# Performance work log

Measured on AMD Instinct MI355X. Metric: run time of the kernel, lower is better.

The kernel has to match this reference:

```python
import jax, jax.numpy as jnp
import numpy as np

BZ = 512      # number of graph pairs
NMAX = 128    # max nodes per graph (pad size; original uses sz.max())
D = 64        # node feature dim
EPS = 1e-3    # sinkhorn entropic regularization (from forward: 0.001)
ITERS = 500   # max_iters (reference runs the full budget, no early stop)
NEG = -1e5    # log(0) surrogate, safe in fp32


def setup_inputs() -> dict:
    key = jax.random.key(0)
    k1, k2, k3, k4 = jax.random.split(key, 4)
    x1 = jax.random.normal(k1, (BZ * NMAX, D), dtype=jnp.float32)
    x2 = jax.random.normal(k2, (BZ * NMAX, D), dtype=jnp.float32)
    # graph sizes in [64, 128] so no empty graphs
    sz1 = jax.random.randint(k3, (BZ,), 64, NMAX + 1, dtype=jnp.int32)
    sz2 = jax.random.randint(k4, (BZ,), 64, NMAX + 1, dtype=jnp.int32)
    return {"x1": x1, "x2": x2, "sz1": sz1, "sz2": sz2}


def _pack(x, sz, nmax):
    """Ragged [total,d] -> padded [bz,nmax,d] plus float mask [bz,nmax].
    Vectorized equivalent of the python packing loop in forward()."""
    off = jnp.cumsum(sz) - sz                       # exclusive prefix sum
    idx = off[:, None] + jnp.arange(nmax)[None, :]  # [bz, nmax]
    mask = jnp.arange(nmax)[None, :] < sz[:, None]
    g = x[jnp.clip(idx, 0, x.shape[0] - 1)] * mask[..., None].astype(x.dtype)
    return g, mask.astype(x.dtype)


def _pairwise_sq(s1, s2):
    """pairwise_distances(set1, set2, p=2): squared euclidean cost [bz,n1,n2]."""
    n1 = jnp.sum(s1 * s1, axis=-1)
    n2 = jnp.sum(s2 * s2, axis=-1)
    M = n1[:, :, None] + n2[:, None, :] - 2.0 * jnp.einsum('bnd,bmd->bnm', s1, s2)
    return jnp.maximum(M, 0.0)


def _sinkhorn(a, b, M, eps, iters):
    """Log-domain entropic Sinkhorn; padded rows/cols have a,b == 0 and
    receive NEG potentials so their transport mass is exp(NEG) ~ 0."""
    la = jnp.where(a > 0, jnp.log(jnp.where(a > 0, a, 1.0)), NEG)
    lb = jnp.where(b > 0, jnp.log(jnp.where(b > 0, b, 1.0)), NEG)
    logK = -M / eps                                  # [bz, n1, n2]

    def body(_, uv):
        u, v = uv
        v = lb - jax.scipy.special.logsumexp(logK + u[:, :, None], axis=1)
        u = la - jax.scipy.special.logsumexp(logK + v[:, None, :], axis=2)
        return (u, v)

    u0 = jnp.zeros_like(a)
    v0 = jnp.zeros_like(b)
    u, v = jax.lax.fori_loop(0, iters, body, (u0, v0))
    return jnp.exp(logK + u[:, :, None] + v[:, None, :])


def reference(x1, x2, sz1, sz2):
    set1, a = _pack(x1, sz1, NMAX)      # [bz, NMAX, D], [bz, NMAX]
    set2, bm = _pack(x2, sz2, NMAX)
    # b = b * a.sum(1,keepdim) / b.sum(1,keepdim)
    b = bm * a.sum(1, keepdims=True) / bm.sum(1, keepdims=True)
    M = _pairwise_sq(set1, set2)
    # original passes M.detach() to sinkhorn -> P is constant w.r.t. grads
    P = _sinkhorn(a, b, jax.lax.stop_gradient(M), EPS, ITERS)
    return jnp.sum(M * P, axis=(1, 2))  # [bz]
```

## Files before the change

### kernel.cpp

```cpp
#include <hip/hip_runtime.h>

#ifndef __has_builtin
#define __has_builtin(x) 0
#endif

typedef float v2f __attribute__((ext_vector_type(2)));

__device__ __forceinline__ float fexp2(float x) {
#if __has_builtin(__builtin_amdgcn_exp2f)
    return __builtin_amdgcn_exp2f(x);
#else
    return exp2f(x);
#endif
}
__device__ __forceinline__ float flog2(float x) {
#if __has_builtin(__builtin_amdgcn_logf)
    return __builtin_amdgcn_logf(x);
#else
    return log2f(x);
#endif
}
__device__ __forceinline__ float frcp(float x) {
#if __has_builtin(__builtin_amdgcn_rcpf)
    return __builtin_amdgcn_rcpf(x);
#else
    return 1.0f / x;
#endif
}

#define DPP_QX1  0xB1
#define DPP_QX2  0x4E
#define DPP_ROR4 0x124
#define DPP_ROR8 0x128

template<int CTRL>
__device__ __forceinline__ float dppf(float x) {
    return __int_as_float(__builtin_amdgcn_update_dpp(
        0, __float_as_int(x), CTRL, 0xF, 0xF, true));
}
__device__ __forceinline__ float swzx16(float x) {
    return __int_as_float(__builtin_amdgcn_ds_swizzle(__float_as_int(x), 0x401F));
}

__device__ __forceinline__ float sel4(float a0, float a1, float a2, float a3,
                                      bool c1, bool c2) {
    float x = c1 ? a1 : a0;
    float y = c1 ? a3 : a2;
    return c2 ? y : x;
}

#define NMAXN 128
#define DD    64
#define MAX_ITERS 500
#define KLOG  12

#define NEG2  (-144269.50408889634f)
#define LKSC  (-1442.6950408889634f)
#define OUTSC (-6.931471805599453e-4f)

#define LK(r, c) (((c) & 1) ? lk2[r][(c) >> 1].y : lk2[r][(c) >> 1].x)

struct SmemStage {
    float A[NMAXN * 33];
    float B[NMAXN * 33];
    float nA[NMAXN];
    float nB[NMAXN];
};
struct SmemSink {
    float2 plog[NMAXN * 10];
    float  ulog[NMAXN];
    float  pmul[NMAXN * 9];
    float  g[NMAXN];
};
union SmemU {
    SmemStage st;
    SmemSink  sk;
    char force[61440];
};

__global__ __launch_bounds__(512, 1)
void balance_kernel(const int* __restrict__ sz1, int* __restrict__ perm)
{
    __shared__ int keys[512];
    const int tid = threadIdx.x;
    const int k = sz1[tid];
    keys[tid] = k;
    __syncthreads();
    int r = 0;
    for (int j = 0; j < 512; ++j) {
        const int kj = keys[j];
        r += (int)((kj < k) | ((kj == k) & (j < tid)));
    }
    const int p = (r < 256) ? r : (767 - r);
    perm[p] = tid;
}

template<int NR>
__device__ __forceinline__ float sink_mul(
    v2f (&lk2)[8][2], const float (&uloc)[8], const float (&v)[4],
    const float (&fm)[4], float gmask,
    SmemU& sm, int rg, int cg, int w, int crow, int q)
{
    const bool c1 = (cg & 1) != 0;
    const bool c2 = (cg & 2) != 0;
    const int  pstoreL = (rg + 16 * cg) * 9 + w;
    const int  pstoreH = pstoreL + 576;

    v2f Q2[NR][2];
#pragma unroll
    for (int r = 0; r < NR; ++r)
#pragma unroll
        for (int j = 0; j < 2; ++j) {
            Q2[r][j].x = fexp2(LK(r, 2*j    ) + uloc[r] + v[2*j    ]);
            Q2[r][j].y = fexp2(LK(r, 2*j + 1) + uloc[r] + v[2*j + 1]);
        }
    float gl[NR];
#pragma unroll
    for (int r = 0; r < NR; ++r) gl[r] = 1.f;
    v2f fc2[2];
    fc2[0].x = fc2[0].y = 0.f;
    fc2[1] = fc2[0];

    for (int k = KLOG; k < MAX_ITERS; ++k) {
        v2f p0 = Q2[0][0] * gl[0];
        v2f q0 = Q2[0][1] * gl[0];
        v2f p1; p1.x = 0.f; p1.y = 0.f;
        v2f q1 = p1;
        if constexpr (NR > 1) { p1 = Q2[1][0] * gl[1]; q1 = Q2[1][1] * gl[1]; }
#pragma unroll
        for (int r = 2; r < NR; ++r) {
            if ((r & 1) == 0) { p0 += Q2[r][0] * gl[r]; q0 += Q2[r][1] * gl[r]; }
            else              { p1 += Q2[r][0] * gl[r]; q1 += Q2[r][1] * gl[r]; }
        }
        v2f s20 = p0 + p1;
        v2f s21 = q0 + q1;
        float s[4] = { s20.x, s20.y, s21.x, s21.y };
#pragma unroll
        for (int c = 0; c < 4; ++c) s[c] += dppf<DPP_ROR4>(s[c]);
#pragma unroll
        for (int c = 0; c < 4; ++c) s[c] += dppf<DPP_ROR8>(s[c]);
#pragma unroll
        for (int c = 0; c < 4; ++c) s[c] += swzx16(s[c]);
#pragma unroll
        for (int c = 0; c < 4; ++c) s[c] += __shfl_xor(s[c], 32);
        fc2[0].x = fm[0] * frcp(fmaxf(s[0], 1e-37f));
        fc2[0].y = fm[1] * frcp(fmaxf(s[1], 1e-37f));
        fc2[1].x = fm[2] * frcp(fmaxf(s[2], 1e-37f));
        fc2[1].y = fm[3] * frcp(fmaxf(s[3], 1e-37f));

        float tr[8];
#pragma unroll
        for (int r = 0; r < NR; ++r) {
            v2f t2 = Q2[r][0] * fc2[0];
            t2 += Q2[r][1] * fc2[1];
            float t = t2.x + t2.y;
            t += dppf<DPP_QX1>(t);
            t += dppf<DPP_QX2>(t);
            tr[r] = t;
        }
        {
            float tlo = sel4(tr[0], tr[1], tr[2], tr[3], c1, c2);
            sm.sk.pmul[pstoreL] = tlo;
            if constexpr (NR > 4) {
                float thi = sel4(tr[4],
                                 (NR > 5) ? tr[5] : tr[4],
                                 (NR > 6) ? tr[6] : tr[4],
                                 (NR > 7) ? tr[7] : tr[4], c1, c2);
                if constexpr (NR == 8) {
                    sm.sk.pmul[pstoreH] = thi;
                } else {
                    if (cg < NR - 4) sm.sk.pmul[pstoreH] = thi;
                }
            }
        }
        __syncthreads();

        {
            float t0 = sm.sk.pmul[crow * 9 + 2 * q];
            float t1 = sm.sk.pmul[crow * 9 + 2 * q + 1];
            float t = t0 + t1;
            t += dppf<DPP_QX1>(t);
            t += dppf<DPP_QX2>(t);
            float gg = gmask * frcp(fmaxf(t, 1e-37f));
            if (q == 0) sm.sk.g[crow] = gg;
        }
        __syncthreads();

#pragma unroll
        for (int r = 0; r < NR; ++r) gl[r] = sm.sk.g[rg + 16*r];

        if ((k & 15) == 15) {
#pragma unroll
            for (int r = 0; r < NR; ++r) {
                Q2[r][0] *= fc2[0] * gl[r];
                Q2[r][1] *= fc2[1] * gl[r];
                gl[r] = 1.f;
            }
        }
    }

    v2f acc2; acc2.x = 0.f; acc2.y = 0.f;
#pragma unroll
    for (int r = 0; r < NR; ++r)
#pragma unroll
        for (int j = 0; j < 2; ++j)
            acc2 += lk2[r][j] * (Q2[r][j] * (fc2[j] * gl[r]));
    return acc2.x + acc2.y;
}

__global__ __launch_bounds__(512, 4)
void wasserstein_kernel(const float* __restrict__ x1, const float* __restrict__ x2,
                        const int* __restrict__ sz1, const int* __restrict__ sz2,
                        const int* __restrict__ perm,
                        float* __restrict__ out)
{
    __shared__ SmemU  sm;
    __shared__ int    soff[16];
    __shared__ float  swred[8];

    const int b    = perm[blockIdx.x];
    const int tid  = threadIdx.x;
    const int w    = tid >> 6;
    const int lane = tid & 63;
    const int rg   = lane >> 2;
    const int cg   = lane & 3;
    const int cb32 = (w << 2) | cg;

    int a1 = (tid < b) ? sz1[tid] : 0;
    int a2 = (tid < b) ? sz2[tid] : 0;
#pragma unroll
    for (int d = 1; d < 64; d <<= 1) {
        a1 += __shfl_xor(a1, d);
        a2 += __shfl_xor(a2, d);
    }
    if (lane == 0) { soff[w] = a1; soff[8 + w] = a2; }
    if (tid < NMAXN) { sm.st.nA[tid] = 0.f; sm.st.nB[tid] = 0.f; }
    __syncthreads();
    int off1 = 0, off2 = 0;
#pragma unroll
    for (int i = 0; i < 8; ++i) { off1 += soff[i]; off2 += soff[8 + i]; }
    const int n1 = sz1[b];
    const int n2 = sz2[b];

    v2f lk2[8][2];
#pragma unroll
    for (int r = 0; r < 8; ++r)
#pragma unroll
        for (int j = 0; j < 2; ++j) { lk2[r][j].x = 0.f; lk2[r][j].y = 0.f; }

    const int srow = tid >> 2;
    const int sq   = tid & 3;

    for (int ch = 0; ch < 2; ++ch) {
        const float* p1 = x1 + (size_t)(off1 + srow) * DD + ch * 32 + sq * 8;
        const float* p2 = x2 + (size_t)(off2 + srow) * DD + ch * 32 + sq * 8;
        const bool ok1 = srow < n1;
        const bool ok2 = srow < n2;
        float va[8], vb[8];
#pragma unroll
        for (int qq = 0; qq < 2; ++qq) {
            float4 t1 = ok1 ? ((const float4*)p1)[qq] : make_float4(0.f, 0.f, 0.f, 0.f);
            float4 t2 = ok2 ? ((const float4*)p2)[qq] : make_float4(0.f, 0.f, 0.f, 0.f);
            va[4*qq+0] = t1.x; va[4*qq+1] = t1.y; va[4*qq+2] = t1.z; va[4*qq+3] = t1.w;
            vb[4*qq+0] = t2.x; vb[4*qq+1] = t2.y; vb[4*qq+2] = t2.z; vb[4*qq+3] = t2.w;
        }
        float s1 = 0.f, s2v = 0.f;
#pragma unroll
        for (int j = 0; j < 8; ++j) {
            sm.st.A[srow * 33 + sq * 8 + j] = va[j];
            sm.st.B[srow * 33 + sq * 8 + j] = vb[j];
            s1  += va[j] * va[j];
            s2v += vb[j] * vb[j];
        }
        s1  += dppf<DPP_QX1>(s1);  s1  += dppf<DPP_QX2>(s1);
        s2v += dppf<DPP_QX1>(s2v); s2v += dppf<DPP_QX2>(s2v);
        if (sq == 0) { sm.st.nA[srow] += s1; sm.st.nB[srow] += s2v; }
        __syncthreads();
#pragma unroll 2
        for (int d = 0; d < 32; ++d) {
            float av[8];
            v2f bv2[2];
#pragma unroll
            for (int r = 0; r < 8; ++r) av[r] = sm.st.A[(rg + 16*r) * 33 + d];
            bv2[0].x = sm.st.B[(cb32     ) * 33 + d];
            bv2[0].y = sm.st.B[(cb32 + 32) * 33 + d];
            bv2[1].x = sm.st.B[(cb32 + 64) * 33 + d];
            bv2[1].y = sm.st.B[(cb32 + 96) * 33 + d];
#pragma unroll
            for (int r = 0; r < 8; ++r)
#pragma unroll
                for (int j = 0; j < 2; ++j)
                    lk2[r][j] += bv2[j] * av[r];
        }
        __syncthreads();
    }

    float lb[4];
    const float lbv = flog2((float)n1) - flog2((float)n2);
    {
        float rn1[8];
        v2f rn2[2];
#pragma unroll
        for (int r = 0; r < 8; ++r) rn1[r] = sm.st.nA[rg + 16*r];
        rn2[0].x = sm.st.nB[cb32];      rn2[0].y = sm.st.nB[cb32 + 32];
        rn2[1].x = sm.st.nB[cb32 + 64]; rn2[1].y = sm.st.nB[cb32 + 96];
#pragma unroll
        for (int r = 0; r < 8; ++r)
#pragma unroll
            for (int j = 0; j < 2; ++j) {
                v2f M2 = rn1[r] + rn2[j] - 2.f * lk2[r][j];
                lk2[r][j].x = fmaxf(M2.x, 0.f) * LKSC;
                lk2[r][j].y = fmaxf(M2.y, 0.f) * LKSC;
            }
#pragma unroll
        for (int c = 0; c < 4; ++c)
            lb[c] = (cb32 + 32*c < n2) ? lbv : NEG2;
    }
    __syncthreads();

    const int   crow   = tid >> 2;
    const int   q      = tid & 3;
    const float lacrow = (crow < n1) ? 0.f : NEG2;

    float uloc[8], v[4];
#pragma unroll
    for (int r = 0; r < 8; ++r) uloc[r] = 0.f;

    for (int k = 0; k < KLOG; ++k) {
        float mx[4], sc[4];
#pragma unroll
        for (int c = 0; c < 4; ++c) mx[c] = LK(0, c) + uloc[0];
#pragma unroll
        for (int r = 1; r < 8; ++r)
#pragma unroll
            for (int c = 0; c < 4; ++c)
                mx[c] = fmaxf(mx[c], LK(r, c) + uloc[r]);
#pragma unroll
        for (int c = 0; c < 4; ++c) mx[c] = fmaxf(mx[c], dppf<DPP_ROR4>(mx[c]));
#pragma unroll
        for (int c = 0; c < 4; ++c) mx[c] = fmaxf(mx[c], dppf<DPP_ROR8>(mx[c]));
#pragma unroll
        for (int c = 0; c < 4; ++c) mx[c] = fmaxf(mx[c], swzx16(mx[c]));
#pragma unroll
        for (int c = 0; c < 4; ++c) mx[c] = fmaxf(mx[c], __shfl_xor(mx[c], 32));
#pragma unroll
        for (int c = 0; c < 4; ++c) sc[c] = fexp2(LK(0, c) + uloc[0] - mx[c]);
#pragma unroll
        for (int r = 1; r < 8; ++r)
#pragma unroll
            for (int c = 0; c < 4; ++c)
                sc[c] += fexp2(LK(r, c) + uloc[r] - mx[c]);
#pragma unroll
        for (int c = 0; c < 4; ++c) sc[c] += dppf<DPP_ROR4>(sc[c]);
#pragma unroll
        for (int c = 0; c < 4; ++c) sc[c] += dppf<DPP_ROR8>(sc[c]);
#pragma unroll
        for (int c = 0; c < 4; ++c) sc[c] += swzx16(sc[c]);
#pragma unroll
        for (int c = 0; c < 4; ++c) sc[c] += __shfl_xor(sc[c], 32);
#pragma unroll
        for (int c = 0; c < 4; ++c)
            v[c] = lb[c] - (mx[c] + flog2(sc[c]));

#pragma unroll
        for (int r = 0; r < 8; ++r) {
            float mr = LK(r, 0) + v[0];
#pragma unroll
            for (int c = 1; c < 4; ++c) mr = fmaxf(mr, LK(r, c) + v[c]);
            mr = fmaxf(mr, dppf<DPP_QX1>(mr));
            mr = fmaxf(mr, dppf<DPP_QX2>(mr));
            float sr = fexp2(LK(r, 0) + v[0] - mr);
#pragma unroll
            for (int c = 1; c < 4; ++c) sr += fexp2(LK(r, c) + v[c] - mr);
            sr += dppf<DPP_QX1>(sr);
            sr += dppf<DPP_QX2>(sr);
            if ((r & 3) == cg)
                sm.sk.plog[(rg + 16*r) * 10 + w] = make_float2(mr, sr);
        }
        __syncthreads();

        {
            float4 t = *(const float4*)&sm.sk.plog[crow * 10 + 2 * q];
            float m = fmaxf(t.x, t.z);
            float s = t.y * fexp2(t.x - m) + t.w * fexp2(t.z - m);
            float mo = dppf<DPP_QX1>(m), so = dppf<DPP_QX1>(s);
            float mm = fmaxf(m, mo);
            s = s * fexp2(m - mm) + so * fexp2(mo - mm); m = mm;
            mo = dppf<DPP_QX2>(m); so = dppf<DPP_QX2>(s);
            mm = fmaxf(m, mo);
            s = s * fexp2(m - mm) + so * fexp2(mo - mm); m = mm;
            if (q == 0) sm.sk.ulog[crow] = lacrow - (m + flog2(s));
        }
        __syncthreads();

#pragma unroll
        for (int r = 0; r < 8; ++r) uloc[r] = sm.sk.ulog[rg + 16*r];
    }

    const float bmulv = (float)n1 / (float)n2;
    float fm[4];
#pragma unroll
    for (int c = 0; c < 4; ++c)
        fm[c] = (cb32 + 32*c < n2) ? bmulv : 0.f;
    const float gmask = (crow < n1) ? 1.f : 0.f;

    float acc;
    const int nr = (n1 + 15) >> 4;
    switch (nr) {
        case 4:  acc = sink_mul<4>(lk2, uloc, v, fm, gmask, sm, rg, cg, w, crow, q); break;
        case 5:  acc = sink_mul<5>(lk2, uloc, v, fm, gmask, sm, rg, cg, w, crow, q); break;
        case 6:  acc = sink_mul<6>(lk2, uloc, v, fm, gmask, sm, rg, cg, w, crow, q); break;
        case 7:  acc = sink_mul<7>(lk2, uloc, v, fm, gmask, sm, rg, cg, w, crow, q); break;
        default: acc = sink_mul<8>(lk2, uloc, v, fm, gmask, sm, rg, cg, w, crow, q); break;
    }

    acc += dppf<DPP_QX1>(acc);
    acc += dppf<DPP_QX2>(acc);
    acc += dppf<DPP_ROR4>(acc);
    acc += dppf<DPP_ROR8>(acc);
    acc += swzx16(acc);
    acc += __shfl_xor(acc, 32);
    if (lane == 0) swred[w] = acc;
    __syncthreads();
    if (tid == 0) {
        float s = 0.f;
#pragma unroll
        for (int i = 0; i < 8; ++i) s += swred[i];
        out[b] = s * OUTSC;
    }
}

extern "C" void kernel_launch(void* const* d_in, const int* in_sizes, int n_in,
                              void* d_out, int out_size, void* d_ws, size_t ws_size,
                              hipStream_t stream) {
    const float* x1  = (const float*)d_in[0];
    const float* x2  = (const float*)d_in[1];
    const int*   sz1 = (const int*)d_in[2];
    const int*   sz2 = (const int*)d_in[3];
    float* out = (float*)d_out;
    int* perm = (int*)d_ws;

    hipLaunchKernelGGL(balance_kernel, dim3(1), dim3(512), 0, stream, sz1, perm);
    hipLaunchKernelGGL(wasserstein_kernel, dim3(512), dim3(512), 0, stream,
                       x1, x2, sz1, sz2, perm, out);
}
```

Baseline: 593.7 us.

## Process two graph pairs per block with interleaved double-buffered Sinkhorn iterations

Each block now handles two graph pairs, taking one from the small half and one from the large half of the balance permutation. Their multiplicative Sinkhorn iterations are interleaved with separate pmul/g buffers, so one pair's reduction latency overlaps with the other's compute. This halves barrier stalls per pair and fills each wave with more independent work. The cost is roughly double the register pressure: launch bounds drop from 4 to 2 blocks per SM, the grid halves to 256 blocks, and the forced shared-memory padding is removed.

```diff
diff --git a/kernel.cpp b/kernel.cpp
--- a/kernel.cpp
+++ b/kernel.cpp
@@ -53,6 +53,7 @@
 #define DD    64
 #define MAX_ITERS 500
 #define KLOG  12
+#define NITER (MAX_ITERS - KLOG)
 
 #define NEG2  (-144269.50408889634f)
 #define LKSC  (-1442.6950408889634f)
@@ -69,13 +70,14 @@
 struct SmemSink {
     float2 plog[NMAXN * 10];
     float  ulog[NMAXN];
-    float  pmul[NMAXN * 9];
-    float  g[NMAXN];
+    float  pmulA[NMAXN * 9];
+    float  pmulB[NMAXN * 9];
+    float  gA[NMAXN];
+    float  gB[NMAXN];
 };
 union SmemU {
     SmemStage st;
     SmemSink  sk;
-    char force[61440];
 };
 
 __global__ __launch_bounds__(512, 1)
@@ -95,137 +97,11 @@
     perm[p] = tid;
 }
 
-template<int NR>
-__device__ __forceinline__ float sink_mul(
-    v2f (&lk2)[8][2], const float (&uloc)[8], const float (&v)[4],
-    const float (&fm)[4], float gmask,
-    SmemU& sm, int rg, int cg, int w, int crow, int q)
-{
-    const bool c1 = (cg & 1) != 0;
-    const bool c2 = (cg & 2) != 0;
-    const int  pstoreL = (rg + 16 * cg) * 9 + w;
-    const int  pstoreH = pstoreL + 576;
-
-    v2f Q2[NR][2];
-#pragma unroll
-    for (int r = 0; r < NR; ++r)
-#pragma unroll
-        for (int j = 0; j < 2; ++j) {
-            Q2[r][j].x = fexp2(LK(r, 2*j    ) + uloc[r] + v[2*j    ]);
-            Q2[r][j].y = fexp2(LK(r, 2*j + 1) + uloc[r] + v[2*j + 1]);
-        }
-    float gl[NR];
-#pragma unroll
-    for (int r = 0; r < NR; ++r) gl[r] = 1.f;
-    v2f fc2[2];
-    fc2[0].x = fc2[0].y = 0.f;
-    fc2[1] = fc2[0];
-
-    for (int k = KLOG; k < MAX_ITERS; ++k) {
-        v2f p0 = Q2[0][0] * gl[0];
-        v2f q0 = Q2[0][1] * gl[0];
-        v2f p1; p1.x = 0.f; p1.y = 0.f;
-        v2f q1 = p1;
-        if constexpr (NR > 1) { p1 = Q2[1][0] * gl[1]; q1 = Q2[1][1] * gl[1]; }
-#pragma unroll
-        for (int r = 2; r < NR; ++r) {
-            if ((r & 1) == 0) { p0 += Q2[r][0] * gl[r]; q0 += Q2[r][1] * gl[r]; }
-            else              { p1 += Q2[r][0] * gl[r]; q1 += Q2[r][1] * gl[r]; }
-        }
-        v2f s20 = p0 + p1;
-        v2f s21 = q0 + q1;
-        float s[4] = { s20.x, s20.y, s21.x, s21.y };
-#pragma unroll
-        for (int c = 0; c < 4; ++c) s[c] += dppf<DPP_ROR4>(s[c]);
-#pragma unroll
-        for (int c = 0; c < 4; ++c) s[c] += dppf<DPP_ROR8>(s[c]);
-#pragma unroll
-        for (int c = 0; c < 4; ++c) s[c] += swzx16(s[c]);
-#pragma unroll
-        for (int c = 0; c < 4; ++c) s[c] += __shfl_xor(s[c], 32);
-        fc2[0].x = fm[0] * frcp(fmaxf(s[0], 1e-37f));
-        fc2[0].y = fm[1] * frcp(fmaxf(s[1], 1e-37f));
-        fc2[1].x = fm[2] * frcp(fmaxf(s[2], 1e-37f));
-        fc2[1].y = fm[3] * frcp(fmaxf(s[3], 1e-37f));
-
-        float tr[8];
-#pragma unroll
-        for (int r = 0; r < NR; ++r) {
-            v2f t2 = Q2[r][0] * fc2[0];
-            t2 += Q2[r][1] * fc2[1];
-            float t = t2.x + t2.y;
-            t += dppf<DPP_QX1>(t);
-            t += dppf<DPP_QX2>(t);
-            tr[r] = t;
-        }
-        {
-            float tlo = sel4(tr[0], tr[1], tr[2], tr[3], c1, c2);
-            sm.sk.pmul[pstoreL] = tlo;
-            if constexpr (NR > 4) {
-                float thi = sel4(tr[4],
-                                 (NR > 5) ? tr[5] : tr[4],
-                                 (NR > 6) ? tr[6] : tr[4],
-                                 (NR > 7) ? tr[7] : tr[4], c1, c2);
-                if constexpr (NR == 8) {
-                    sm.sk.pmul[pstoreH] = thi;
-                } else {
-                    if (cg < NR - 4) sm.sk.pmul[pstoreH] = thi;
-                }
-            }
-        }
-        __syncthreads();
-
-        {
-            float t0 = sm.sk.pmul[crow * 9 + 2 * q];
-            float t1 = sm.sk.pmul[crow * 9 + 2 * q + 1];
-            float t = t0 + t1;
-            t += dppf<DPP_QX1>(t);
-            t += dppf<DPP_QX2>(t);
-            float gg = gmask * frcp(fmaxf(t, 1e-37f));
-            if (q == 0) sm.sk.g[crow] = gg;
-        }
-        __syncthreads();
-
-#pragma unroll
-        for (int r = 0; r < NR; ++r) gl[r] = sm.sk.g[rg + 16*r];
-
-        if ((k & 15) == 15) {
-#pragma unroll
-            for (int r = 0; r < NR; ++r) {
-                Q2[r][0] *= fc2[0] * gl[r];
-                Q2[r][1] *= fc2[1] * gl[r];
-                gl[r] = 1.f;
-            }
-        }
-    }
-
-    v2f acc2; acc2.x = 0.f; acc2.y = 0.f;
-#pragma unroll
-    for (int r = 0; r < NR; ++r)
-#pragma unroll
-        for (int j = 0; j < 2; ++j)
-            acc2 += lk2[r][j] * (Q2[r][j] * (fc2[j] * gl[r]));
-    return acc2.x + acc2.y;
-}
-
-__global__ __launch_bounds__(512, 4)
-void wasserstein_kernel(const float* __restrict__ x1, const float* __restrict__ x2,
-                        const int* __restrict__ sz1, const int* __restrict__ sz2,
-                        const int* __restrict__ perm,
-                        float* __restrict__ out)
-{
-    __shared__ SmemU  sm;
-    __shared__ int    soff[16];
-    __shared__ float  swred[8];
-
-    const int b    = perm[blockIdx.x];
-    const int tid  = threadIdx.x;
-    const int w    = tid >> 6;
-    const int lane = tid & 63;
-    const int rg   = lane >> 2;
-    const int cg   = lane & 3;
-    const int cb32 = (w << 2) | cg;
-
+__device__ __forceinline__ void prefix_off(const int* __restrict__ sz1,
+                                           const int* __restrict__ sz2,
+                                           int b, int tid, int w, int lane,
+                                           int* soff, int& off1, int& off2)
+{
     int a1 = (tid < b) ? sz1[tid] : 0;
     int a2 = (tid < b) ? sz2[tid] : 0;
 #pragma unroll
@@ -234,19 +110,25 @@
         a2 += __shfl_xor(a2, d);
     }
     if (lane == 0) { soff[w] = a1; soff[8 + w] = a2; }
+    __syncthreads();
+    off1 = 0; off2 = 0;
+#pragma unroll
+    for (int i = 0; i < 8; ++i) { off1 += soff[i]; off2 += soff[8 + i]; }
+    __syncthreads();
+}
+
+__device__ __forceinline__ void stage_pair(
+    const float* __restrict__ x1, const float* __restrict__ x2,
+    int off1, int off2, int n1, int n2, SmemU& sm,
+    int tid, int rg, int cb32, v2f (&lk2)[8][2])
+{
+#pragma unroll
+    for (int r = 0; r < 8; ++r)
+#pragma unroll
+        for (int j = 0; j < 2; ++j) { lk2[r][j].x = 0.f; lk2[r][j].y = 0.f; }
+
     if (tid < NMAXN) { sm.st.nA[tid] = 0.f; sm.st.nB[tid] = 0.f; }
     __syncthreads();
-    int off1 = 0, off2 = 0;
-#pragma unroll
-    for (int i = 0; i < 8; ++i) { off1 += soff[i]; off2 += soff[8 + i]; }
-    const int n1 = sz1[b];
-    const int n2 = sz2[b];
-
-    v2f lk2[8][2];
-#pragma unroll
-    for (int r = 0; r < 8; ++r)
-#pragma unroll
-        for (int j = 0; j < 2; ++j) { lk2[r][j].x = 0.f; lk2[r][j].y = 0.f; }
 
     const int srow = tid >> 2;
     const int sq   = tid & 3;
@@ -295,8 +177,6 @@
         __syncthreads();
     }
 
-    float lb[4];
-    const float lbv = flog2((float)n1) - flog2((float)n2);
     {
         float rn1[8];
         v2f rn2[2];
@@ -312,17 +192,21 @@
                 lk2[r][j].x = fmaxf(M2.x, 0.f) * LKSC;
                 lk2[r][j].y = fmaxf(M2.y, 0.f) * LKSC;
             }
-#pragma unroll
-        for (int c = 0; c < 4; ++c)
-            lb[c] = (cb32 + 32*c < n2) ? lbv : NEG2;
     }
     __syncthreads();
-
-    const int   crow   = tid >> 2;
-    const int   q      = tid & 3;
+}
+
+__device__ __forceinline__ void phase1(
+    v2f (&lk2)[8][2], int n1, int n2, SmemU& sm,
+    int rg, int cg, int w, int cb32, int crow, int q,
+    float (&uloc)[8], float (&v)[4])
+{
+    float lb[4];
+    const float lbv = flog2((float)n1) - flog2((float)n2);
+#pragma unroll
+    for (int c = 0; c < 4; ++c)
+        lb[c] = (cb32 + 32*c < n2) ? lbv : NEG2;
     const float lacrow = (crow < n1) ? 0.f : NEG2;
-
-    float uloc[8], v[4];
 #pragma unroll
     for (int r = 0; r < 8; ++r) uloc[r] = 0.f;
 
@@ -396,37 +280,265 @@
 #pragma unroll
         for (int r = 0; r < 8; ++r) uloc[r] = sm.sk.ulog[rg + 16*r];
     }
-
-    const float bmulv = (float)n1 / (float)n2;
-    float fm[4];
-#pragma unroll
-    for (int c = 0; c < 4; ++c)
-        fm[c] = (cb32 + 32*c < n2) ? bmulv : 0.f;
-    const float gmask = (crow < n1) ? 1.f : 0.f;
-
-    float acc;
-    const int nr = (n1 + 15) >> 4;
-    switch (nr) {
-        case 4:  acc = sink_mul<4>(lk2, uloc, v, fm, gmask, sm, rg, cg, w, crow, q); break;
-        case 5:  acc = sink_mul<5>(lk2, uloc, v, fm, gmask, sm, rg, cg, w, crow, q); break;
-        case 6:  acc = sink_mul<6>(lk2, uloc, v, fm, gmask, sm, rg, cg, w, crow, q); break;
-        case 7:  acc = sink_mul<7>(lk2, uloc, v, fm, gmask, sm, rg, cg, w, crow, q); break;
-        default: acc = sink_mul<8>(lk2, uloc, v, fm, gmask, sm, rg, cg, w, crow, q); break;
-    }
-
-    acc += dppf<DPP_QX1>(acc);
-    acc += dppf<DPP_QX2>(acc);
-    acc += dppf<DPP_ROR4>(acc);
-    acc += dppf<DPP_ROR8>(acc);
-    acc += swzx16(acc);
-    acc += __shfl_xor(acc, 32);
-    if (lane == 0) swred[w] = acc;
+}
+
+template<int NR>
+__device__ __forceinline__ void mul_compute(
+    v2f (&Q2)[NR][2], const float (&gl)[NR], v2f (&fc2)[2],
+    const float (&fm)[4], float* __restrict__ pmul,
+    int pstoreL, int pstoreH, bool c1, bool c2, int cg)
+{
+    v2f p0 = Q2[0][0] * gl[0];
+    v2f q0 = Q2[0][1] * gl[0];
+    v2f p1; p1.x = 0.f; p1.y = 0.f;
+    v2f q1 = p1;
+    if constexpr (NR > 1) { p1 = Q2[1][0] * gl[1]; q1 = Q2[1][1] * gl[1]; }
+#pragma unroll
+    for (int r = 2; r < NR; ++r) {
+        if ((r & 1) == 0) { p0 += Q2[r][0] * gl[r]; q0 += Q2[r][1] * gl[r]; }
+        else              { p1 += Q2[r][0] * gl[r]; q1 += Q2[r][1] * gl[r]; }
+    }
+    v2f s20 = p0 + p1;
+    v2f s21 = q0 + q1;
+    float s[4] = { s20.x, s20.y, s21.x, s21.y };
+#pragma unroll
+    for (int c = 0; c < 4; ++c) s[c] += dppf<DPP_ROR4>(s[c]);
+#pragma unroll
+    for (int c = 0; c < 4; ++c) s[c] += dppf<DPP_ROR8>(s[c]);
+#pragma unroll
+    for (int c = 0; c < 4; ++c) s[c] += swzx16(s[c]);
+#pragma unroll
+    for (int c = 0; c < 4; ++c) s[c] += __shfl_xor(s[c], 32);
+    fc2[0].x = fm[0] * frcp(fmaxf(s[0], 1e-37f));
+    fc2[0].y = fm[1] * frcp(fmaxf(s[1], 1e-37f));
+    fc2[1].x = fm[2] * frcp(fmaxf(s[2], 1e-37f));
+    fc2[1].y = fm[3] * frcp(fmaxf(s[3], 1e-37f));
+
+    float tr[8];
+#pragma unroll
+    for (int r = 0; r < NR; ++r) {
+        v2f t2 = Q2[r][0] * fc2[0];
+        t2 += Q2[r][1] * fc2[1];
+        float t = t2.x + t2.y;
+        t += dppf<DPP_QX1>(t);
+        t += dppf<DPP_QX2>(t);
+        tr[r] = t;
+    }
+    float tlo = sel4(tr[0], tr[1], tr[2], tr[3], c1, c2);
+    pmul[pstoreL] = tlo;
+    if constexpr (NR > 4) {
+        float thi = sel4(tr[4],
+                         (NR > 5) ? tr[5] : tr[4],
+                         (NR > 6) ? tr[6] : tr[4],
+                         (NR > 7) ? tr[7] : tr[4], c1, c2);
+        if constexpr (NR == 8) {
+            pmul[pstoreH] = thi;
+        } else {
+            if (cg < NR - 4) pmul[pstoreH] = thi;
+        }
+    }
+}
+
+__device__ __forceinline__ void mul_combine(
+    float t0, float t1, float gmask, float* __restrict__ gdst, int crow, int q)
+{
+    float t = t0 + t1;
+    t += dppf<DPP_QX1>(t);
+    t += dppf<DPP_QX2>(t);
+    float gg = gmask * frcp(fmaxf(t, 1e-37f));
+    if (q == 0) gdst[crow] = gg;
+}
+
+template<int NR>
+__device__ __forceinline__ void fold_pair(v2f (&Q2)[NR][2], float (&gl)[NR],
+                                          const v2f (&fc2)[2])
+{
+#pragma unroll
+    for (int r = 0; r < NR; ++r) {
+        Q2[r][0] *= fc2[0] * gl[r];
+        Q2[r][1] *= fc2[1] * gl[r];
+        gl[r] = 1.f;
+    }
+}
+
+template<int NRS>
+__device__ __forceinline__ void sink2(
+    v2f (&lkA)[8][2], const float (&uA)[8], const float (&vA)[4],
+    const float (&fmA)[4], float gmaskA,
+    v2f (&lkB)[8][2], const float (&uB)[8], const float (&vB)[4],
+    const float (&fmB)[4], float gmaskB,
+    SmemU& sm, int rg, int cg, int w, int crow, int q,
+    float& accA, float& accB)
+{
+    const bool c1 = (cg & 1) != 0;
+    const bool c2 = (cg & 2) != 0;
+    const int  pstoreL = (rg + 16 * cg) * 9 + w;
+    const int  pstoreH = pstoreL + 576;
+    const int  pread   = crow * 9 + 2 * q;
+
+    v2f QA[NRS][2];
+    {
+        v2f (&lk2)[8][2] = lkA;
+#pragma unroll
+        for (int r = 0; r < NRS; ++r)
+#pragma unroll
+            for (int j = 0; j < 2; ++j) {
+                QA[r][j].x = fexp2(LK(r, 2*j    ) + uA[r] + vA[2*j    ]);
+                QA[r][j].y = fexp2(LK(r, 2*j + 1) + uA[r] + vA[2*j + 1]);
+            }
+    }
+    v2f QB[8][2];
+    {
+        v2f (&lk2)[8][2] = lkB;
+#pragma unroll
+        for (int r = 0; r < 8; ++r)
+#pragma unroll
+            for (int j = 0; j < 2; ++j) {
+                QB[r][j].x = fexp2(LK(r, 2*j    ) + uB[r] + vB[2*j    ]);
+                QB[r][j].y = fexp2(LK(r, 2*j + 1) + uB[r] + vB[2*j + 1]);
+            }
+    }
+
+    float glA[NRS], glB[8];
+#pragma unroll
+    for (int r = 0; r < NRS; ++r) glA[r] = 1.f;
+#pragma unroll
+    for (int r = 0; r < 8; ++r) glB[r] = 1.f;
+    v2f fcA[2], fcB[2];
+    fcA[0].x = fcA[0].y = 0.f; fcA[1] = fcA[0];
+    fcB[0] = fcA[0]; fcB[1] = fcA[0];
+
+    for (int i = 0; i < NITER; ++i) {
+        const int k = i + KLOG;
+        float tB0 = sm.sk.pmulB[pread];
+        float tB1 = sm.sk.pmulB[pread + 1];
+        mul_compute<NRS>(QA, glA, fcA, fmA, sm.sk.pmulA, pstoreL, pstoreH, c1, c2, cg);
+        if (i > 0)
+            mul_combine(tB0, tB1, gmaskB, sm.sk.gB, crow, q);
+        __syncthreads();
+        if (i > 0) {
+#pragma unroll
+            for (int r = 0; r < 8; ++r) glB[r] = sm.sk.gB[rg + 16*r];
+            if (((k - 1) & 15) == 15) fold_pair<8>(QB, glB, fcB);
+        }
+        float tA0 = sm.sk.pmulA[pread];
+        float tA1 = sm.sk.pmulA[pread + 1];
+        mul_compute<8>(QB, glB, fcB, fmB, sm.sk.pmulB, pstoreL, pstoreH, c1, c2, cg);
+        mul_combine(tA0, tA1, gmaskA, sm.sk.gA, crow, q);
+        __syncthreads();
+#pragma unroll
+        for (int r = 0; r < NRS; ++r) glA[r] = sm.sk.gA[rg + 16*r];
+        if ((k & 15) == 15) fold_pair<NRS>(QA, glA, fcA);
+    }
+
+    {
+        float tB0 = sm.sk.pmulB[pread];
+        float tB1 = sm.sk.pmulB[pread + 1];
+        mul_combine(tB0, tB1, gmaskB, sm.sk.gB, crow, q);
+        __syncthreads();
+#pragma unroll
+        for (int r = 0; r < 8; ++r) glB[r] = sm.sk.gB[rg + 16*r];
+    }
+
+    v2f a2; a2.x = 0.f; a2.y = 0.f;
+#pragma unroll
+    for (int r = 0; r < NRS; ++r)
+#pragma unroll
+        for (int j = 0; j < 2; ++j)
+            a2 += lkA[r][j] * (QA[r][j] * (fcA[j] * glA[r]));
+    accA = a2.x + a2.y;
+    v2f b2; b2.x = 0.f; b2.y = 0.f;
+#pragma unroll
+    for (int r = 0; r < 8; ++r)
+#pragma unroll
+        for (int j = 0; j < 2; ++j)
+            b2 += lkB[r][j] * (QB[r][j] * (fcB[j] * glB[r]));
+    accB = b2.x + b2.y;
+}
+
+__global__ __launch_bounds__(512, 2)
+void wasserstein_kernel(const float* __restrict__ x1, const float* __restrict__ x2,
+                        const int* __restrict__ sz1, const int* __restrict__ sz2,
+                        const int* __restrict__ perm,
+                        float* __restrict__ out)
+{
+    __shared__ SmemU  sm;
+    __shared__ int    soff[16];
+    __shared__ float  swredA[8];
+    __shared__ float  swredB[8];
+
+    const int blk  = blockIdx.x;
+    const int bA   = perm[blk];
+    const int bB   = perm[blk + 256];
+    const int tid  = threadIdx.x;
+    const int w    = tid >> 6;
+    const int lane = tid & 63;
+    const int rg   = lane >> 2;
+    const int cg   = lane & 3;
+    const int cb32 = (w << 2) | cg;
+    const int crow = tid >> 2;
+    const int q    = tid & 3;
+
+    int off1A, off2A, off1B, off2B;
+    prefix_off(sz1, sz2, bA, tid, w, lane, soff, off1A, off2A);
+    prefix_off(sz1, sz2, bB, tid, w, lane, soff, off1B, off2B);
+    const int n1A = sz1[bA], n2A = sz2[bA];
+    const int n1B = sz1[bB], n2B = sz2[bB];
+
+    v2f lkA[8][2], lkB[8][2];
+    stage_pair(x1, x2, off1A, off2A, n1A, n2A, sm, tid, rg, cb32, lkA);
+    stage_pair(x1, x2, off1B, off2B, n1B, n2B, sm, tid, rg, cb32, lkB);
+
+    float uA[8], vA[4], uB[8], vB[4];
+    phase1(lkA, n1A, n2A, sm, rg, cg, w, cb32, crow, q, uA, vA);
+    phase1(lkB, n1B, n2B, sm, rg, cg, w, cb32, crow, q, uB, vB);
+
+    float fmA[4], fmB[4];
+    const float bmA = (float)n1A / (float)n2A;
+    const float bmB = (float)n1B / (float)n2B;
+#pragma unroll
+    for (int c = 0; c < 4; ++c) {
+        fmA[c] = (cb32 + 32*c < n2A) ? bmA : 0.f;
+        fmB[c] = (cb32 + 32*c < n2B) ? bmB : 0.f;
+    }
+    const float gmaskA = (crow < n1A) ? 1.f : 0.f;
+    const float gmaskB = (crow < n1B) ? 1.f : 0.f;
+
+    float accA, accB;
+    const int nrS = (n1A + 15) >> 4;
+    switch (nrS) {
+        case 4:  sink2<4>(lkA, uA, vA, fmA, gmaskA, lkB, uB, vB, fmB, gmaskB,
+                          sm, rg, cg, w, crow, q, accA, accB); break;
+        case 5:  sink2<5>(lkA, uA, vA, fmA, gmaskA, lkB, uB, vB, fmB, gmaskB,
+                          sm, rg, cg, w, crow, q, accA, accB); break;
+        case 6:  sink2<6>(lkA, uA, vA, fmA, gmaskA, lkB, uB, vB, fmB, gmaskB,
+                          sm, rg, cg, w, crow, q, accA, accB); break;
+        case 7:  sink2<7>(lkA, uA, vA, fmA, gmaskA, lkB, uB, vB, fmB, gmaskB,
+                          sm, rg, cg, w, crow, q, accA, accB); break;
+        default: sink2<8>(lkA, uA, vA, fmA, gmaskA, lkB, uB, vB, fmB, gmaskB,
+                          sm, rg, cg, w, crow, q, accA, accB); break;
+    }
+
+    accA += dppf<DPP_QX1>(accA);
+    accA += dppf<DPP_QX2>(accA);
+    accA += dppf<DPP_ROR4>(accA);
+    accA += dppf<DPP_ROR8>(accA);
+    accA += swzx16(accA);
+    accA += __shfl_xor(accA, 32);
+    accB += dppf<DPP_QX1>(accB);
+    accB += dppf<DPP_QX2>(accB);
+    accB += dppf<DPP_ROR4>(accB);
+    accB += dppf<DPP_ROR8>(accB);
+    accB += swzx16(accB);
+    accB += __shfl_xor(accB, 32);
+    if (lane == 0) { swredA[w] = accA; swredB[w] = accB; }
     __syncthreads();
     if (tid == 0) {
-        float s = 0.f;
-#pragma unroll
-        for (int i = 0; i < 8; ++i) s += swred[i];
-        out[b] = s * OUTSC;
+        float sA = 0.f, sB = 0.f;
+#pragma unroll
+        for (int i = 0; i < 8; ++i) { sA += swredA[i]; sB += swredB[i]; }
+        out[bA] = sA * OUTSC;
+        out[bB] = sB * OUTSC;
     }
 }
 
@@ -441,6 +553,6 @@
     int* perm = (int*)d_ws;
 
     hipLaunchKernelGGL(balance_kernel, dim3(1), dim3(512), 0, stream, sz1, perm);
-    hipLaunchKernelGGL(wasserstein_kernel, dim3(512), dim3(512), 0, stream,
+    hipLaunchKernelGGL(wasserstein_kernel, dim3(256), dim3(512), 0, stream,
                        x1, x2, sz1, sz2, perm, out);
 }
```

New measurement: 745.1 us. 25.5% more time.
